# Optimization experiments

Hardware: AMD Instinct MI355X
Metric: run time of the kernel (lower is better)

## Reference

```python
import jax, jax.numpy as jnp
import numpy as np

PC_MIN = jnp.array([0.0, -39.68, -3.0], jnp.float32)
VOX = jnp.array([0.16, 0.16, 4.0], jnp.float32)
NX, NY = 432, 496  # grid cells in x and y (z grid size is 1)
MAXP = 32          # max points per pillar


def setup_inputs():
    key = jax.random.key(0)
    ks = jax.random.split(key, 16)
    B, N = 2, 16000
    u = jax.random.uniform(ks[0], (B, N, 4), dtype=jnp.float32)
    # points uniformly spread over the point-cloud range, intensity in [0,1)
    points = jnp.stack([u[..., 0] * 69.12, u[..., 1] * 79.36 - 39.68,
                        u[..., 2] * 4.0 - 3.0, u[..., 3]], axis=-1)

    def cw(k, co, ci):
        return jax.random.normal(k, (co, ci, 3, 3), jnp.float32) / np.float32(np.sqrt(ci * 9.0))

    def cws(k, L, c):
        return jax.random.normal(k, (L, c, c, 3, 3), jnp.float32) / np.float32(np.sqrt(c * 9.0))

    def st(k, shape):
        k1, k2 = jax.random.split(k)
        return (1.0 + 0.1 * jax.random.normal(k1, shape, jnp.float32),
                0.1 * jax.random.normal(k2, shape, jnp.float32))

    vfe_w = 0.1 * jax.random.normal(ks[1], (64, 10), jnp.float32)
    vfe_s, vfe_t = st(ks[2], (64,))
    b1_w0 = cw(ks[3], 4, 64);   b1_s0, b1_t0 = st(ks[4], (4,))
    b1_w = cws(ks[5], 3, 4);    b1_s, b1_t = st(ks[6], (3, 4))
    b2_w0 = cw(ks[7], 16, 4);   b2_s0, b2_t0 = st(ks[8], (16,))
    b2_w = cws(ks[9], 5, 16);   b2_s, b2_t = st(ks[10], (5, 16))
    b3_w0 = cw(ks[11], 64, 16); b3_s0, b3_t0 = st(ks[12], (64,))
    b3_w = cws(ks[13], 5, 64);  b3_s, b3_t = st(ks[14], (5, 64))
    return dict(points=points, vfe_w=vfe_w, vfe_s=vfe_s, vfe_t=vfe_t,
                b1_w0=b1_w0, b1_s0=b1_s0, b1_t0=b1_t0, b1_w=b1_w, b1_s=b1_s, b1_t=b1_t,
                b2_w0=b2_w0, b2_s0=b2_s0, b2_t0=b2_t0, b2_w=b2_w, b2_s=b2_s, b2_t=b2_t,
                b3_w0=b3_w0, b3_s0=b3_s0, b3_t0=b3_t0, b3_w=b3_w, b3_s=b3_s, b3_t=b3_t)


def _voxelize_vfe_scatter(points, vfe_w, vfe_s, vfe_t):
    """Hard voxelization (hash-bucket by pillar coord, pad to MAXP) + PillarVFE + scatter to BEV canvas."""
    B, N, C = points.shape
    V = B * N  # worst case: every point its own pillar
    pts = points.reshape(V, C)
    cid = jnp.floor((pts[:, :3] - PC_MIN) / VOX).astype(jnp.int32)
    cid = jnp.clip(cid, 0, jnp.array([NX - 1, NY - 1, 0], jnp.int32))
    bidx = jnp.repeat(jnp.arange(B, dtype=jnp.int32), N)
    # linear pillar id: b*NY*NX + y*NX + x  (z grid dim is 1 -> z idx always 0)
    gid = bidx * (NY * NX) + cid[:, 1] * NX + cid[:, 0]
    order = jnp.argsort(gid)  # stable -> preserves per-pillar point order
    g = gid[order]; p = pts[order]; c = cid[order]
    pos = jnp.arange(V, dtype=jnp.int32)
    flag = jnp.concatenate([jnp.ones((1,), bool), g[1:] != g[:-1]])
    vidx = jnp.cumsum(flag) - 1                                 # dense pillar index
    rank = pos - jax.lax.cummax(jnp.where(flag, pos, 0), axis=0)  # slot within pillar
    keep = rank < MAXP
    voxels = jnp.zeros((V, MAXP, C), points.dtype).at[vidx, rank].set(p, mode='drop')
    num = jnp.zeros((V,), jnp.int32).at[vidx].add(keep.astype(jnp.int32))
    OOB = B * NY * NX
    pillar_gid = jnp.full((V,), OOB, jnp.int32).at[vidx].set(g)  # unused slots stay out-of-bounds
    pillar_c = jnp.zeros((V, 3), jnp.int32).at[vidx].set(c)
    # PillarVFE features: [x,y,z,r, cluster offset(3), center offset(3)] = 10
    denom = jnp.maximum(num, 1).astype(points.dtype)[:, None]
    mean = jnp.zeros((V, 3), points.dtype).at[vidx].add(p[:, :3] * keep[:, None]) / denom
    f_cluster = voxels[:, :, :3] - mean[:, None, :]
    center = pillar_c.astype(points.dtype) * VOX + (VOX * 0.5 + PC_MIN)
    f_center = voxels[:, :, :3] - center[:, None, :]
    mask = (jnp.arange(MAXP)[None, :] < num[:, None])[:, :, None].astype(points.dtype)
    feat = jnp.concatenate([voxels, f_cluster, f_center], axis=-1) * mask  # (V, 32, 10)
    x = jnp.einsum('vpc,oc->vpo', feat, vfe_w)        # PFN linear (no bias)
    x = jax.nn.relu(x * vfe_s + vfe_t)                # eval-mode BN folded to scale/shift
    pillar = x.max(axis=1)                            # (V, 64) max over points
    canvas = jnp.zeros((B * NY * NX, 64), points.dtype).at[pillar_gid].set(pillar, mode='drop')
    return canvas.reshape(B, NY, NX, 64).transpose(0, 3, 1, 2)  # (B, 64, NY, NX)


def _conv_bn_relu(x, w, s, t):
    y = jax.lax.conv_general_dilated(x, w, (1, 1), [(1, 1), (1, 1)],
                                     dimension_numbers=('NCHW', 'OIHW', 'NCHW'))
    return jax.nn.relu(y * s[None, :, None, None] + t[None, :, None, None])


def _block(x, w0, s0, t0, ws, ss, ts):
    x = _conv_bn_relu(x, w0, s0, t0)
    for i in range(ws.shape[0]):  # fixed small layer count
        x = _conv_bn_relu(x, ws[i], ss[i], ts[i])
    return x


def reference(points, vfe_w, vfe_s, vfe_t,
              b1_w0, b1_s0, b1_t0, b1_w, b1_s, b1_t,
              b2_w0, b2_s0, b2_t0, b2_w, b2_s, b2_t,
              b3_w0, b3_s0, b3_t0, b3_w, b3_s, b3_t):
    bev = _voxelize_vfe_scatter(points, vfe_w, vfe_s, vfe_t)
    x1 = _block(bev, b1_w0, b1_s0, b1_t0, b1_w, b1_s, b1_t)
    x2 = _block(x1, b2_w0, b2_s0, b2_t0, b2_w, b2_s, b2_t)
    x3 = _block(x2, b3_w0, b3_s0, b3_t0, b3_w, b3_s, b3_t)
    # no deblocks (cfg lacks UPSAMPLE_STRIDES) -> concat raw block outputs: 4+16+64 = 84 ch
    return jnp.concatenate([x1, x2, x3], axis=1)  # (B, 84, 496, 432)
```

## Files before the change

### kernel.cpp

```cpp
#include <hip/hip_runtime.h>
#include <math.h>

static constexpr int H = 496, W = 432, Bn = 2, Np = 16000;
static constexpr int HW = H * W;

typedef __bf16 bf16x8 __attribute__((ext_vector_type(8)));
typedef float f32x16 __attribute__((ext_vector_type(16)));

__device__ inline void bin_xy(float px, float py, int& ix, int& iy) {
  ix = (int)floorf(px * 6.25f);
  iy = (int)floorf((py + 39.68f) * 6.25f);
  ix = min(max(ix, 0), W - 1);
  iy = min(max(iy, 0), H - 1);
}

__global__ __launch_bounds__(256)
void count_kernel(const float* __restrict__ pts, int* __restrict__ cnt,
                  float* __restrict__ sums) {
  int p = blockIdx.x * blockDim.x + threadIdx.x;
  if (p >= Bn * Np) return;
  float px = pts[p * 4 + 0], py = pts[p * 4 + 1], pz = pts[p * 4 + 2];
  int b = p / Np;
  int ix, iy;
  bin_xy(px, py, ix, iy);
  int gid = b * HW + iy * W + ix;
  atomicAdd(&cnt[gid], 1);
  atomicAdd(&sums[3 * gid + 0], px);
  atomicAdd(&sums[3 * gid + 1], py);
  atomicAdd(&sums[3 * gid + 2], pz);
}

__global__ __launch_bounds__(256)
void vfe_kernel(const float* __restrict__ pts, const int* __restrict__ cnt,
                const float* __restrict__ sums, const float* __restrict__ vw,
                const float* __restrict__ vs, const float* __restrict__ vt,
                float* __restrict__ canv) {
  int tid = blockIdx.x * blockDim.x + threadIdx.x;
  if (tid >= Bn * Np * 64) return;
  int o = tid & 63;
  int p = tid >> 6;
  int b = p / Np;
  float px = pts[p * 4 + 0], py = pts[p * 4 + 1];
  float pz = pts[p * 4 + 2], pr = pts[p * 4 + 3];
  int ix, iy;
  bin_xy(px, py, ix, iy);
  int gid = b * HW + iy * W + ix;
  int n = cnt[gid];
  float denom = (float)max(n, 1);
  float mx = sums[3 * gid + 0] / denom;
  float my = sums[3 * gid + 1] / denom;
  float mz = sums[3 * gid + 2] / denom;
  float cx = (float)ix * 0.16f + 0.08f;
  float cy = (float)iy * 0.16f + (0.08f - 39.68f);
  float f[10] = {px, py, pz, pr, px - mx, py - my, pz - mz,
                 px - cx, py - cy, pz + 1.0f};
  const float* wr = vw + o * 10;
  float d = 0.f;
#pragma unroll
  for (int c = 0; c < 10; c++) d += f[c] * wr[c];
  float val = d * vs[o] + vt[o];
  val = fmaxf(val, 0.f);
  if (n < 32) val = fmaxf(val, fmaxf(vt[o], 0.f));
  unsigned int* dst = (unsigned int*)(canv + (size_t)gid * 64 + o);
  atomicMax(dst, __float_as_uint(val));
}

__global__ __launch_bounds__(128, 2)
void conv64_tile(const float* __restrict__ canv, const float* __restrict__ wc,
                 const float* __restrict__ s, const float* __restrict__ t,
                 float* __restrict__ out4) {
  __shared__ __align__(16) float hl[180 * 64];

  const int tid = threadIdx.x;
  const int b = blockIdx.y;
  const int ty = blockIdx.x / 27, tx = blockIdx.x - ty * 27;
  const int y0 = ty * 8, x0 = tx * 16;
  const float* cb = canv + (size_t)b * HW * 64;

  for (int q = tid; q < 180 * 16; q += 128) {
    int hp = q >> 4, c4 = q & 15;
    int hy = hp / 18, hx = hp - hy * 18;
    int gy = y0 - 1 + hy, gx = x0 - 1 + hx;
    float4 v = {0.f, 0.f, 0.f, 0.f};
    if ((unsigned)gy < (unsigned)H && (unsigned)gx < (unsigned)W)
      v = *(const float4*)(cb + (size_t)(gy * W + gx) * 64 + c4 * 4);
    *(float4*)(hl + hp * 64 + ((c4 + hp) & 15) * 4) = v;
  }
  __syncthreads();

  const int ly = tid >> 4, lx = tid & 15;
  float a0 = 0.f, a1 = 0.f, a2 = 0.f, a3 = 0.f;

#pragma unroll 1
  for (int tp = 0; tp < 9; ++tp) {
    const int hp = (ly + tp / 3) * 18 + lx + tp % 3;
    const float* hb = hl + hp * 64;
    const float* wt_ = wc + tp * 256;
#pragma unroll 4
    for (int c4 = 0; c4 < 16; ++c4) {
      float4 v = *(const float4*)(hb + ((c4 + hp) & 15) * 4);
      float4 wq0 = *(const float4*)(wt_ + (c4 * 4 + 0) * 4);
      float4 wq1 = *(const float4*)(wt_ + (c4 * 4 + 1) * 4);
      float4 wq2 = *(const float4*)(wt_ + (c4 * 4 + 2) * 4);
      float4 wq3 = *(const float4*)(wt_ + (c4 * 4 + 3) * 4);
      a0 = fmaf(v.x, wq0.x, a0);
      a1 = fmaf(v.x, wq0.y, a1);
      a2 = fmaf(v.x, wq0.z, a2);
      a3 = fmaf(v.x, wq0.w, a3);
      a0 = fmaf(v.y, wq1.x, a0);
      a1 = fmaf(v.y, wq1.y, a1);
      a2 = fmaf(v.y, wq1.z, a2);
      a3 = fmaf(v.y, wq1.w, a3);
      a0 = fmaf(v.z, wq2.x, a0);
      a1 = fmaf(v.z, wq2.y, a1);
      a2 = fmaf(v.z, wq2.z, a2);
      a3 = fmaf(v.z, wq2.w, a3);
      a0 = fmaf(v.w, wq3.x, a0);
      a1 = fmaf(v.w, wq3.y, a1);
      a2 = fmaf(v.w, wq3.z, a2);
      a3 = fmaf(v.w, wq3.w, a3);
    }
  }
  float* ob = out4 + (size_t)b * 4 * HW + (size_t)(y0 + ly) * W + x0 + lx;
  ob[0 * HW] = fmaxf(a0 * s[0] + t[0], 0.f);
  ob[1 * HW] = fmaxf(a1 * s[1] + t[1], 0.f);
  ob[2 * HW] = fmaxf(a2 * s[2] + t[2], 0.f);
  ob[3 * HW] = fmaxf(a3 * s[3] + t[3], 0.f);
}

template <int CI, int COT>
__global__ __launch_bounds__(256)
void conv3x3(const float* __restrict__ in, int in_bs, const float* __restrict__ w,
             const float* __restrict__ s, const float* __restrict__ t,
             float* __restrict__ out, int out_bs, int npix) {
  int pix = blockIdx.x * blockDim.x + threadIdx.x;
  if (pix >= npix) return;
  int b = pix / HW;
  int rem = pix - b * HW;
  int y = rem / W;
  int x = rem - y * W;
  int co0 = blockIdx.y * COT;
  const float* inb = in + (size_t)b * in_bs;

  int offs[9];
  bool okm[9];
#pragma unroll
  for (int ky = 0; ky < 3; ky++) {
    int yy = y + ky - 1;
    bool yok = (unsigned)yy < (unsigned)H;
#pragma unroll
    for (int kx = 0; kx < 3; kx++) {
      int xx = x + kx - 1;
      okm[ky * 3 + kx] = yok && ((unsigned)xx < (unsigned)W);
      offs[ky * 3 + kx] = yy * W + xx;
    }
  }
  float acc[COT];
#pragma unroll
  for (int i = 0; i < COT; i++) acc[i] = 0.f;
  for (int ci = 0; ci < CI; ci++) {
    const float* ip = inb + (size_t)ci * HW;
    float iv[9];
#pragma unroll
    for (int k = 0; k < 9; k++) iv[k] = okm[k] ? ip[offs[k]] : 0.f;
    const float* wp = w + ((size_t)co0 * CI + ci) * 9;
#pragma unroll
    for (int cg_ = 0; cg_ < COT; cg_++) {
      const float* wc_ = wp + (size_t)cg_ * CI * 9;
#pragma unroll
      for (int k = 0; k < 9; k++) acc[cg_] = fmaf(iv[k], wc_[k], acc[cg_]);
    }
  }
  float* ob = out + (size_t)b * out_bs + (size_t)rem;
#pragma unroll
  for (int cg_ = 0; cg_ < COT; cg_++) {
    float v = acc[cg_] * s[co0 + cg_] + t[co0 + cg_];
    ob[(size_t)(co0 + cg_) * HW] = fmaxf(v, 0.f);
  }
}

__global__ __launch_bounds__(256)
void conv16_dual(const float* __restrict__ in, const float* __restrict__ w,
                 const float* __restrict__ s, const float* __restrict__ t,
                 float* __restrict__ out, __bf16* __restrict__ n16) {
  int pix = blockIdx.x * blockDim.x + threadIdx.x;
  if (pix >= Bn * HW) return;
  int b = pix / HW;
  int rem = pix - b * HW;
  int y = rem / W;
  int x = rem - y * W;
  const float* inb = in + (size_t)b * 16 * HW;

  int offs[9];
  bool okm[9];
#pragma unroll
  for (int ky = 0; ky < 3; ky++) {
    int yy = y + ky - 1;
    bool yok = (unsigned)yy < (unsigned)H;
#pragma unroll
    for (int kx = 0; kx < 3; kx++) {
      int xx = x + kx - 1;
      okm[ky * 3 + kx] = yok && ((unsigned)xx < (unsigned)W);
      offs[ky * 3 + kx] = yy * W + xx;
    }
  }
  float acc[16];
#pragma unroll
  for (int i = 0; i < 16; i++) acc[i] = 0.f;
  for (int ci = 0; ci < 16; ci++) {
    const float* ip = inb + (size_t)ci * HW;
    float iv[9];
#pragma unroll
    for (int k = 0; k < 9; k++) iv[k] = okm[k] ? ip[offs[k]] : 0.f;
    const float* wp = w + (size_t)ci * 9;
#pragma unroll
    for (int cg_ = 0; cg_ < 16; cg_++) {
      const float* wc_ = wp + (size_t)cg_ * 16 * 9;
#pragma unroll
      for (int k = 0; k < 9; k++) acc[cg_] = fmaf(iv[k], wc_[k], acc[cg_]);
    }
  }
  float* ob = out + (size_t)b * 84 * HW + (size_t)rem;
  __bf16 vv[16];
#pragma unroll
  for (int cg_ = 0; cg_ < 16; cg_++) {
    float v = fmaxf(acc[cg_] * s[cg_] + t[cg_], 0.f);
    ob[(size_t)cg_ * HW] = v;
    vv[cg_] = (__bf16)v;
  }
  __bf16* nb = n16 + (size_t)b * (84 * HW * 2) + (size_t)rem * 16;
  *(bf16x8*)nb = *(bf16x8*)vv;
  *(bf16x8*)(nb + 8) = *(bf16x8*)(vv + 8);
}

__global__ __launch_bounds__(256)
void prepack(const float* __restrict__ w0, const float* __restrict__ ws,
             __bf16* __restrict__ wt, const float* __restrict__ w1,
             float* __restrict__ wc) {
  int idx = blockIdx.x * 256 + threadIdx.x;
  const int E0 = 64 * 144, EN = 64 * 576;
  if (idx < E0) {
    int blk = idx >> 9, rem = idx & 511;
    int tp = blk >> 1, nt = blk & 1;
    int co = nt * 32 + (rem >> 4);
    int ci = rem & 15;
    int ky = tp / 3, kx = tp - ky * 3;
    wt[idx] = (__bf16)w0[((co * 16 + ci) * 3 + ky) * 3 + kx];
  } else if (idx < E0 + 5 * EN) {
    int j = idx - E0;
    int n = j / EN, rr = j - n * EN;
    int blk = rr >> 9, rem = rr & 511;
    int tpkc = blk >> 1, nt = blk & 1;
    int tp = tpkc >> 2, kc = tpkc & 3;
    int co = nt * 32 + (rem >> 4);
    int ci = kc * 16 + (rem & 15);
    int ky = tp / 3, kx = tp - ky * 3;
    wt[idx] = (__bf16)ws[n * 36864 + ((co * 64 + ci) * 3 + ky) * 3 + kx];
  } else if (idx < E0 + 5 * EN + 2304) {
    int e = idx - E0 - 5 * EN;
    int tp = e >> 8, r = e & 255;
    int ci = r >> 2, co = r & 3;
    wc[e] = w1[co * 576 + ci * 9 + tp];
  }
}

template <int CI, bool FINAL>
__global__ __launch_bounds__(256, 3)
void mconv(const __bf16* __restrict__ in, size_t in_bstride,
           const __bf16* __restrict__ wt, const float* __restrict__ s,
           const float* __restrict__ t, __bf16* __restrict__ outb,
           size_t outb_bstride, float* __restrict__ outf, size_t outf_bstride) {
  constexpr int KC = CI / 16;
  constexpr int PADW = (CI == 64) ? 72 : 24;
  constexpr int HALO_B = 324 * PADW * 2;
  constexpr int TRAN_B = FINAL ? 128 * 66 * 4 : 0;
  constexpr int SMEM_B = HALO_B > TRAN_B ? HALO_B : TRAN_B;
  __shared__ __align__(16) char smem[SMEM_B];
  __bf16* hl = (__bf16*)smem;

  const int tid = threadIdx.x;
  const int bz = blockIdx.y;
  const int ty = blockIdx.x / 27, tx = blockIdx.x - ty * 27;
  const int y0 = ty * 16, x0 = tx * 16;
  in += (size_t)bz * in_bstride;

  constexpr int NCH = CI / 8;
  constexpr int TOT = 324 * NCH;
  for (int q = tid; q < TOT; q += 256) {
    int hp = q / NCH, c8 = q - hp * NCH;
    int hy = hp / 18, hx = hp - hy * 18;
    int gy = y0 - 1 + hy, gx = x0 - 1 + hx;
    int4 v = {0, 0, 0, 0};
    if ((unsigned)gy < (unsigned)H && (unsigned)gx < (unsigned)W)
      v = *(const int4*)(in + (size_t)(gy * W + gx) * CI + c8 * 8);
    *(int4*)(hl + hp * PADW + c8 * 8) = v;
  }
  __syncthreads();

  const int lane = tid & 63;
  const int wv = tid >> 6;
  const int col = lane & 31, half = lane >> 5;
  const int ly0 = 4 * wv + (col >> 4);
  const int lx = col & 15;

  f32x16 z = {0.f, 0.f, 0.f, 0.f, 0.f, 0.f, 0.f, 0.f,
              0.f, 0.f, 0.f, 0.f, 0.f, 0.f, 0.f, 0.f};
  f32x16 a00 = z, a01 = z, a10 = z, a11 = z;

  const int laneoff = col * 16 + half * 8;
  const __bf16* wbase = wt + laneoff;

#pragma unroll
  for (int tp = 0; tp < 9; ++tp) {
    const __bf16* a0r = hl + ((ly0 + tp / 3) * 18 + lx + tp % 3) * PADW + half * 8;
    const __bf16* a1r = a0r + 2 * 18 * PADW;
    const __bf16* bb = wbase + ((tp * KC) << 10);
#pragma unroll
    for (int kc = 0; kc < KC; ++kc) {
      bf16x8 af0 = *(const bf16x8*)(a0r + kc * 16);
      bf16x8 af1 = *(const bf16x8*)(a1r + kc * 16);
      bf16x8 b0 = *(const bf16x8*)(bb + (kc << 10));
      bf16x8 b1 = *(const bf16x8*)(bb + (kc << 10) + 512);
      a00 = __builtin_amdgcn_mfma_f32_32x32x16_bf16(af0, b0, a00, 0, 0, 0);
      a01 = __builtin_amdgcn_mfma_f32_32x32x16_bf16(af0, b1, a01, 0, 0, 0);
      a10 = __builtin_amdgcn_mfma_f32_32x32x16_bf16(af1, b0, a10, 0, 0, 0);
      a11 = __builtin_amdgcn_mfma_f32_32x32x16_bf16(af1, b1, a11, 0, 0, 0);
    }
  }

  float s0 = s[col], t0v = t[col], s1 = s[col + 32], t1v = t[col + 32];
  if constexpr (!FINAL) {
    __bf16* ob = outb + (size_t)bz * outb_bstride;
#pragma unroll
    for (int r = 0; r < 16; ++r) {
      int row = (r & 3) + 8 * (r >> 2) + 4 * half;
      int py = y0 + 4 * wv + (row >> 4);
      int px = x0 + (row & 15);
      size_t gp0 = (size_t)py * W + px;
      size_t gp1 = gp0 + (size_t)2 * W;
      ob[gp0 * 64 + col] = (__bf16)fmaxf(a00[r] * s0 + t0v, 0.f);
      ob[gp0 * 64 + col + 32] = (__bf16)fmaxf(a01[r] * s1 + t1v, 0.f);
      ob[gp1 * 64 + col] = (__bf16)fmaxf(a10[r] * s0 + t0v, 0.f);
      ob[gp1 * 64 + col + 32] = (__bf16)fmaxf(a11[r] * s1 + t1v, 0.f);
    }
  } else {
    float* of = outf + (size_t)bz * outf_bstride;
    float* tl = (float*)smem;
    for (int h = 0; h < 2; ++h) {
      __syncthreads();
      if ((wv >> 1) == h) {
        int wl_ = wv & 1;
#pragma unroll
        for (int r = 0; r < 16; ++r) {
          int row = (r & 3) + 8 * (r >> 2) + 4 * half;
          int lp0 = (4 * wl_ + (row >> 4)) * 16 + (row & 15);
          int lp1 = lp0 + 32;
          tl[lp0 * 66 + col] = fmaxf(a00[r] * s0 + t0v, 0.f);
          tl[lp0 * 66 + col + 32] = fmaxf(a01[r] * s1 + t1v, 0.f);
          tl[lp1 * 66 + col] = fmaxf(a10[r] * s0 + t0v, 0.f);
          tl[lp1 * 66 + col + 32] = fmaxf(a11[r] * s1 + t1v, 0.f);
        }
      }
      __syncthreads();
      for (int e = tid; e < 128 * 64; e += 256) {
        int co = e >> 7, mtl = e & 127;
        of[(size_t)co * HW + (size_t)(y0 + h * 8 + (mtl >> 4)) * W +
           (x0 + (mtl & 15))] = tl[mtl * 66 + co];
      }
    }
  }
}

extern "C" void kernel_launch(void* const* d_in, const int* in_sizes, int n_in,
                              void* d_out, int out_size, void* d_ws, size_t ws_size,
                              hipStream_t stream) {
  const float* pts  = (const float*)d_in[0];
  const float* vw   = (const float*)d_in[1];
  const float* vs   = (const float*)d_in[2];
  const float* vt   = (const float*)d_in[3];
  const float* b1w0 = (const float*)d_in[4];
  const float* b1s0 = (const float*)d_in[5];
  const float* b1t0 = (const float*)d_in[6];
  const float* b1w  = (const float*)d_in[7];
  const float* b1s  = (const float*)d_in[8];
  const float* b1t  = (const float*)d_in[9];
  const float* b2w0 = (const float*)d_in[10];
  const float* b2s0 = (const float*)d_in[11];
  const float* b2t0 = (const float*)d_in[12];
  const float* b2w  = (const float*)d_in[13];
  const float* b2s  = (const float*)d_in[14];
  const float* b2t  = (const float*)d_in[15];
  const float* b3w0 = (const float*)d_in[16];
  const float* b3s0 = (const float*)d_in[17];
  const float* b3t0 = (const float*)d_in[18];
  const float* b3w  = (const float*)d_in[19];
  const float* b3s  = (const float*)d_in[20];
  const float* b3t  = (const float*)d_in[21];
  float* out = (float*)d_out;

  float* wsf = (float*)d_ws;
  int* cnt = (int*)wsf;
  float* sums = wsf + (size_t)2 * HW;
  float* s16a = wsf;
  float* s16b = wsf + (size_t)32 * HW;
  float* canv = wsf + (size_t)64 * HW;
  __bf16* ppA = (__bf16*)d_ws;
  __bf16* Wt = (__bf16*)((char*)d_ws + (size_t)192 * HW * 4);
  float* wc64 = (float*)((char*)d_ws + (size_t)192 * HW * 4 + 512 * 1024);

  prepack<<<765, 256, 0, stream>>>(b3w0, b3w, Wt, b1w0, wc64);

  hipMemsetAsync(cnt, 0, (size_t)8 * HW * sizeof(float), stream);
  hipMemsetAsync(canv, 0, (size_t)128 * HW * sizeof(float), stream);

  count_kernel<<<(Bn * Np + 255) / 256, 256, 0, stream>>>(pts, cnt, sums);
  vfe_kernel<<<(Bn * Np * 64 + 255) / 256, 256, 0, stream>>>(pts, cnt, sums, vw, vs,
                                                             vt, canv);

  const int g2 = (2 * HW + 255) / 256;
  dim3 blk(256);

  conv64_tile<<<dim3(27 * 62, Bn), dim3(128), 0, stream>>>(canv, wc64, b1s0, b1t0,
                                                           s16a);
  conv3x3<4, 4><<<dim3(g2, 1), blk, 0, stream>>>(s16a, 4 * HW, b1w + 0 * 144,
                                                 b1s + 0, b1t + 0, s16b, 4 * HW,
                                                 2 * HW);
  conv3x3<4, 4><<<dim3(g2, 1), blk, 0, stream>>>(s16b, 4 * HW, b1w + 1 * 144,
                                                 b1s + 4, b1t + 4, s16a, 4 * HW,
                                                 2 * HW);
  conv3x3<4, 4><<<dim3(g2, 1), blk, 0, stream>>>(s16a, 4 * HW, b1w + 2 * 144,
                                                 b1s + 8, b1t + 8, out, 84 * HW,
                                                 2 * HW);

  __bf16* n16 = (__bf16*)(out + (size_t)20 * HW);
  conv3x3<4, 16><<<dim3(g2, 1), blk, 0, stream>>>(out, 84 * HW, b2w0, b2s0, b2t0,
                                                  s16a, 16 * HW, 2 * HW);
  conv3x3<16, 16><<<dim3(g2, 1), blk, 0, stream>>>(s16a, 16 * HW, b2w + 0 * 2304,
                                                   b2s + 0, b2t + 0, s16b, 16 * HW,
                                                   2 * HW);
  conv3x3<16, 16><<<dim3(g2, 1), blk, 0, stream>>>(s16b, 16 * HW, b2w + 1 * 2304,
                                                   b2s + 16, b2t + 16, s16a, 16 * HW,
                                                   2 * HW);
  conv3x3<16, 16><<<dim3(g2, 1), blk, 0, stream>>>(s16a, 16 * HW, b2w + 2 * 2304,
                                                   b2s + 32, b2t + 32, s16b, 16 * HW,
                                                   2 * HW);
  conv3x3<16, 16><<<dim3(g2, 1), blk, 0, stream>>>(s16b, 16 * HW, b2w + 3 * 2304,
                                                   b2s + 48, b2t + 48, s16a, 16 * HW,
                                                   2 * HW);
  conv16_dual<<<g2, blk, 0, stream>>>(s16a, b2w + 4 * 2304, b2s + 64, b2t + 64,
                                      out + 4 * HW, n16);

  const size_t canv_s = (size_t)84 * HW * 2;
  const size_t ppa_s = (size_t)64 * HW;
  dim3 mg(31 * 27, Bn);
  mconv<16, false><<<mg, blk, 0, stream>>>(n16, canv_s, Wt, b3s0, b3t0, ppA, ppa_s,
                                           nullptr, 0);
  mconv<64, false><<<mg, blk, 0, stream>>>(ppA, ppa_s, Wt + 9216 + 0 * 36864,
                                           b3s + 0, b3t + 0, n16, canv_s, nullptr,
                                           0);
  mconv<64, false><<<mg, blk, 0, stream>>>(n16, canv_s, Wt + 9216 + 1 * 36864,
                                           b3s + 64, b3t + 64, ppA, ppa_s, nullptr,
                                           0);
  mconv<64, false><<<mg, blk, 0, stream>>>(ppA, ppa_s, Wt + 9216 + 2 * 36864,
                                           b3s + 128, b3t + 128, n16, canv_s,
                                           nullptr, 0);
  mconv<64, false><<<mg, blk, 0, stream>>>(n16, canv_s, Wt + 9216 + 3 * 36864,
                                           b3s + 192, b3t + 192, ppA, ppa_s,
                                           nullptr, 0);
  mconv<64, true><<<mg, blk, 0, stream>>>(ppA, ppa_s, Wt + 9216 + 4 * 36864,
                                          b3s + 256, b3t + 256, nullptr, 0,
                                          out + (size_t)20 * HW, (size_t)84 * HW);
}
```

Measured before the change: 818.0 us.

## Split conv64 output channels across waves and stage mconv weights in LDS

The first 64->4 conv now runs 256 threads per tile. Each pair of waves computes two output channels instead of one thread computing all four, which raises parallelism and cuts per-thread register and weight-load pressure. The bf16 MFMA conv now copies each K-chunk's weights for all nine taps into shared memory before the MFMA loop, instead of reading B fragments from global memory, and drops its occupancy hint from 3 to 2. This adds extra barriers per K-chunk and more LDS use in exchange for cheaper weight reads.

```diff
diff --git a/kernel.cpp b/kernel.cpp
--- a/kernel.cpp
+++ b/kernel.cpp
@@ -65,7 +65,7 @@
   atomicMax(dst, __float_as_uint(val));
 }
 
-__global__ __launch_bounds__(128, 2)
+__global__ __launch_bounds__(256, 3)
 void conv64_tile(const float* __restrict__ canv, const float* __restrict__ wc,
                  const float* __restrict__ s, const float* __restrict__ t,
                  float* __restrict__ out4) {
@@ -77,7 +77,7 @@
   const int y0 = ty * 8, x0 = tx * 16;
   const float* cb = canv + (size_t)b * HW * 64;
 
-  for (int q = tid; q < 180 * 16; q += 128) {
+  for (int q = tid; q < 180 * 16; q += 256) {
     int hp = q >> 4, c4 = q & 15;
     int hy = hp / 18, hx = hp - hy * 18;
     int gy = y0 - 1 + hy, gx = x0 - 1 + hx;
@@ -88,44 +88,39 @@
   }
   __syncthreads();
 
-  const int ly = tid >> 4, lx = tid & 15;
-  float a0 = 0.f, a1 = 0.f, a2 = 0.f, a3 = 0.f;
+  const int wv = tid >> 6, lane = tid & 63;
+  const int cp = wv >> 1;
+  const int p = (wv & 1) * 64 + lane;
+  const int ly = p >> 4, lx = p & 15;
+  const int co = cp * 2;
+  float a0 = 0.f, a1 = 0.f;
 
 #pragma unroll 1
   for (int tp = 0; tp < 9; ++tp) {
     const int hp = (ly + tp / 3) * 18 + lx + tp % 3;
     const float* hb = hl + hp * 64;
-    const float* wt_ = wc + tp * 256;
+    const float* wt_ = wc + tp * 256 + co;
 #pragma unroll 4
     for (int c4 = 0; c4 < 16; ++c4) {
       float4 v = *(const float4*)(hb + ((c4 + hp) & 15) * 4);
-      float4 wq0 = *(const float4*)(wt_ + (c4 * 4 + 0) * 4);
-      float4 wq1 = *(const float4*)(wt_ + (c4 * 4 + 1) * 4);
-      float4 wq2 = *(const float4*)(wt_ + (c4 * 4 + 2) * 4);
-      float4 wq3 = *(const float4*)(wt_ + (c4 * 4 + 3) * 4);
-      a0 = fmaf(v.x, wq0.x, a0);
-      a1 = fmaf(v.x, wq0.y, a1);
-      a2 = fmaf(v.x, wq0.z, a2);
-      a3 = fmaf(v.x, wq0.w, a3);
-      a0 = fmaf(v.y, wq1.x, a0);
-      a1 = fmaf(v.y, wq1.y, a1);
-      a2 = fmaf(v.y, wq1.z, a2);
-      a3 = fmaf(v.y, wq1.w, a3);
-      a0 = fmaf(v.z, wq2.x, a0);
-      a1 = fmaf(v.z, wq2.y, a1);
-      a2 = fmaf(v.z, wq2.z, a2);
-      a3 = fmaf(v.z, wq2.w, a3);
-      a0 = fmaf(v.w, wq3.x, a0);
-      a1 = fmaf(v.w, wq3.y, a1);
-      a2 = fmaf(v.w, wq3.z, a2);
-      a3 = fmaf(v.w, wq3.w, a3);
+      const float* wp = wt_ + c4 * 16;
+      float2 w0 = *(const float2*)(wp + 0);
+      float2 w1 = *(const float2*)(wp + 4);
+      float2 w2 = *(const float2*)(wp + 8);
+      float2 w3 = *(const float2*)(wp + 12);
+      a0 = fmaf(v.x, w0.x, a0);
+      a1 = fmaf(v.x, w0.y, a1);
+      a0 = fmaf(v.y, w1.x, a0);
+      a1 = fmaf(v.y, w1.y, a1);
+      a0 = fmaf(v.z, w2.x, a0);
+      a1 = fmaf(v.z, w2.y, a1);
+      a0 = fmaf(v.w, w3.x, a0);
+      a1 = fmaf(v.w, w3.y, a1);
     }
   }
   float* ob = out4 + (size_t)b * 4 * HW + (size_t)(y0 + ly) * W + x0 + lx;
-  ob[0 * HW] = fmaxf(a0 * s[0] + t[0], 0.f);
-  ob[1 * HW] = fmaxf(a1 * s[1] + t[1], 0.f);
-  ob[2 * HW] = fmaxf(a2 * s[2] + t[2], 0.f);
-  ob[3 * HW] = fmaxf(a3 * s[3] + t[3], 0.f);
+  ob[(size_t)co * HW] = fmaxf(a0 * s[co] + t[co], 0.f);
+  ob[(size_t)(co + 1) * HW] = fmaxf(a1 * s[co + 1] + t[co + 1], 0.f);
 }
 
 template <int CI, int COT>
@@ -265,7 +260,7 @@
 }
 
 template <int CI, bool FINAL>
-__global__ __launch_bounds__(256, 3)
+__global__ __launch_bounds__(256, 2)
 void mconv(const __bf16* __restrict__ in, size_t in_bstride,
            const __bf16* __restrict__ wt, const float* __restrict__ s,
            const float* __restrict__ t, __bf16* __restrict__ outb,
@@ -274,9 +269,11 @@
   constexpr int PADW = (CI == 64) ? 72 : 24;
   constexpr int HALO_B = 324 * PADW * 2;
   constexpr int TRAN_B = FINAL ? 128 * 66 * 4 : 0;
-  constexpr int SMEM_B = HALO_B > TRAN_B ? HALO_B : TRAN_B;
+  constexpr int HT_B = HALO_B > TRAN_B ? HALO_B : TRAN_B;
+  constexpr int SMEM_B = HT_B + 18432;
   __shared__ __align__(16) char smem[SMEM_B];
   __bf16* hl = (__bf16*)smem;
+  __bf16* wb = (__bf16*)(smem + HT_B);
 
   const int tid = threadIdx.x;
   const int bz = blockIdx.y;
@@ -295,7 +292,6 @@
       v = *(const int4*)(in + (size_t)(gy * W + gx) * CI + c8 * 8);
     *(int4*)(hl + hp * PADW + c8 * 8) = v;
   }
-  __syncthreads();
 
   const int lane = tid & 63;
   const int wv = tid >> 6;
@@ -308,19 +304,25 @@
   f32x16 a00 = z, a01 = z, a10 = z, a11 = z;
 
   const int laneoff = col * 16 + half * 8;
-  const __bf16* wbase = wt + laneoff;
-
-#pragma unroll
-  for (int tp = 0; tp < 9; ++tp) {
-    const __bf16* a0r = hl + ((ly0 + tp / 3) * 18 + lx + tp % 3) * PADW + half * 8;
-    const __bf16* a1r = a0r + 2 * 18 * PADW;
-    const __bf16* bb = wbase + ((tp * KC) << 10);
-#pragma unroll
-    for (int kc = 0; kc < KC; ++kc) {
-      bf16x8 af0 = *(const bf16x8*)(a0r + kc * 16);
-      bf16x8 af1 = *(const bf16x8*)(a1r + kc * 16);
-      bf16x8 b0 = *(const bf16x8*)(bb + (kc << 10));
-      bf16x8 b1 = *(const bf16x8*)(bb + (kc << 10) + 512);
+
+  for (int kc = 0; kc < KC; ++kc) {
+    if (kc) __syncthreads();
+    for (int q = tid; q < 1152; q += 256) {
+      int tp = q >> 7, wi = (q & 127) * 8;
+      *(int4*)(wb + tp * 1024 + wi) =
+          *(const int4*)(wt + ((tp * KC + kc) << 10) + wi);
+    }
+    __syncthreads();
+#pragma unroll
+    for (int tp = 0; tp < 9; ++tp) {
+      const __bf16* a0r =
+          hl + ((ly0 + tp / 3) * 18 + lx + tp % 3) * PADW + half * 8 + kc * 16;
+      const __bf16* a1r = a0r + 2 * 18 * PADW;
+      const __bf16* bb = wb + tp * 1024 + laneoff;
+      bf16x8 af0 = *(const bf16x8*)a0r;
+      bf16x8 af1 = *(const bf16x8*)a1r;
+      bf16x8 b0 = *(const bf16x8*)bb;
+      bf16x8 b1 = *(const bf16x8*)(bb + 512);
       a00 = __builtin_amdgcn_mfma_f32_32x32x16_bf16(af0, b0, a00, 0, 0, 0);
       a01 = __builtin_amdgcn_mfma_f32_32x32x16_bf16(af0, b1, a01, 0, 0, 0);
       a10 = __builtin_amdgcn_mfma_f32_32x32x16_bf16(af1, b0, a10, 0, 0, 0);
@@ -420,8 +422,7 @@
   const int g2 = (2 * HW + 255) / 256;
   dim3 blk(256);
 
-  conv64_tile<<<dim3(27 * 62, Bn), dim3(128), 0, stream>>>(canv, wc64, b1s0, b1t0,
-                                                           s16a);
+  conv64_tile<<<dim3(27 * 62, Bn), blk, 0, stream>>>(canv, wc64, b1s0, b1t0, s16a);
   conv3x3<4, 4><<<dim3(g2, 1), blk, 0, stream>>>(s16a, 4 * HW, b1w + 0 * 144,
                                                  b1s + 0, b1t + 0, s16b, 4 * HW,
                                                  2 * HW);
```

New measurement: 1.017 ms. 24.4% more time.
